# Kernel tuning notes

Hardware: AMD Instinct MI355X
Metric: run time of the kernel (lower is better)

The kernel has to match this reference:

```python
import jax, jax.numpy as jnp
import numpy as np

B, S, D, H, DH, L, F, V, C = 2, 4096, 768, 12, 64, 2, 3072, 50265, 256
NB = S // C
NEG = -1e9


def layer_norm(x, g, b, eps=1e-5):
    m = jnp.mean(x, -1, keepdims=True)
    v = jnp.mean((x - m) ** 2, -1, keepdims=True)
    return (x - m) * jax.lax.rsqrt(v + eps) * g + b


def _blockify(t):
    # t: [B,H,S,DH] -> [B,H,NB,3C,DH], key blocks (b-1, b, b+1) per query block
    tp = jnp.pad(t, ((0, 0), (0, 0), (C, C), (0, 0)))
    tb = tp.reshape(t.shape[0], t.shape[1], NB + 2, C, DH)
    return jnp.concatenate([tb[:, :, :-2], tb[:, :, 1:-1], tb[:, :, 2:]], axis=3)


def sw_attention(x, mask, Wq, bq, Wk, bk, Wv, bv, Wo, bo):
    Bq = x.shape[0]
    def heads(w, b):
        return (x @ w + b).reshape(Bq, S, H, DH).transpose(0, 2, 1, 3)
    q = heads(Wq, bq) / jnp.sqrt(jnp.float32(DH))
    k = heads(Wk, bk)
    v = heads(Wv, bv)
    qb = q.reshape(Bq, H, NB, C, DH)
    k3, v3 = _blockify(k), _blockify(v)
    scores = jnp.einsum('bhncd,bhnkd->bhnck', qb, k3)  # [B,H,NB,C,3C]
    cc = jnp.arange(C)[:, None]
    kk = jnp.arange(3 * C)[None, :]
    band = (kk >= cc) & (kk <= cc + 2 * C)  # exact |i-j| <= 256 sliding window
    lm = mask.at[:, 0].set(0.0)  # global (CLS) key handled separately, not in band
    mp = jnp.pad(lm, ((0, 0), (C, C))).reshape(Bq, NB + 2, C)
    m3 = jnp.concatenate([mp[:, :-2], mp[:, 1:-1], mp[:, 2:]], axis=2)  # [B,NB,3C]
    valid = band[None, None, None] & (m3[:, None, :, None, :] > 0)
    scores = jnp.where(valid, scores, NEG)
    gk, gv = k[:, :, 0, :], v[:, :, 0, :]  # CLS global key/value
    gsc = jnp.einsum('bhncd,bhd->bhnc', qb, gk)[..., None]  # [B,H,NB,C,1]
    gmask = (mask[:, 0] > 0).reshape(Bq, 1, 1, 1, 1)
    gsc = jnp.where(gmask, gsc, NEG)
    probs = jax.nn.softmax(jnp.concatenate([scores, gsc], -1), -1)
    ctx = (jnp.einsum('bhnck,bhnkd->bhncd', probs[..., :3 * C], v3)
           + probs[..., 3 * C:] * gv[:, :, None, None, :])
    ctx = ctx.reshape(Bq, H, S, DH)
    # CLS is a global query: full attention over all keys
    s0 = jnp.einsum('bhd,bhsd->bhs', q[:, :, 0, :], k)
    s0 = jnp.where(mask[:, None, :] > 0, s0, NEG)
    o0 = jnp.einsum('bhs,bhsd->bhd', jax.nn.softmax(s0, -1), v)
    ctx = ctx.at[:, :, 0, :].set(o0)
    out = ctx.transpose(0, 2, 1, 3).reshape(Bq, S, D)
    return out @ Wo + bo


def setup_inputs() -> dict:
    key = jax.random.key(0)
    ks = jax.random.split(key, 16)
    def w(k, shape, s=0.02):
        return (jax.random.normal(k, shape) * s).astype(jnp.float32)
    return {
        'input_ids': jax.random.randint(ks[0], (B, S), 0, V, dtype=jnp.int32),
        'attention_mask': jnp.ones((B, S), dtype=jnp.int32),
        'emb_tok': w(ks[1], (V, D)),
        'emb_pos': w(ks[2], (S, D)),
        'emb_ln_g': jnp.ones((D,), jnp.float32),
        'emb_ln_b': jnp.zeros((D,), jnp.float32),
        'Wq': w(ks[3], (L, D, D)), 'bq': jnp.zeros((L, D), jnp.float32),
        'Wk': w(ks[4], (L, D, D)), 'bk': jnp.zeros((L, D), jnp.float32),
        'Wv': w(ks[5], (L, D, D)), 'bv': jnp.zeros((L, D), jnp.float32),
        'Wo': w(ks[6], (L, D, D)), 'bo': jnp.zeros((L, D), jnp.float32),
        'ln1_g': jnp.ones((L, D), jnp.float32), 'ln1_b': jnp.zeros((L, D), jnp.float32),
        'W1': w(ks[7], (L, D, F)), 'b1': jnp.zeros((L, F), jnp.float32),
        'W2': w(ks[8], (L, F, D)), 'b2': jnp.zeros((L, D), jnp.float32),
        'ln2_g': jnp.ones((L, D), jnp.float32), 'ln2_b': jnp.zeros((L, D), jnp.float32),
        'cls_W': w(ks[9], (D, 3)), 'cls_b': jnp.zeros((3,), jnp.float32),
    }


def reference(input_ids, attention_mask, emb_tok, emb_pos, emb_ln_g, emb_ln_b,
              Wq, bq, Wk, bk, Wv, bv, Wo, bo, ln1_g, ln1_b,
              W1, b1, W2, b2, ln2_g, ln2_b, cls_W, cls_b):
    mask = attention_mask.astype(jnp.float32)
    h = layer_norm(emb_tok[input_ids] + emb_pos[None], emb_ln_g, emb_ln_b)
    for l in range(L):
        a = sw_attention(h, mask, Wq[l], bq[l], Wk[l], bk[l], Wv[l], bv[l], Wo[l], bo[l])
        h = layer_norm(h + a, ln1_g[l], ln1_b[l])
        f = jax.nn.gelu(h @ W1[l] + b1[l], approximate=False) @ W2[l] + b2[l]
        h = layer_norm(h + f, ln2_g[l], ln2_b[l])
    logits = h[:, 0] @ cls_W + cls_b  # dropout is identity at inference
    return logits
```

## Files before the change

### kernel.cpp

```cpp
#include <hip/hip_runtime.h>
#include <math.h>

#define BB 2
#define SS 4096
#define DD 768
#define HH 12
#define LL 2
#define FF 3072
#define CC 256
#define MM 8192
#define QB 128

using frag8 = __attribute__((ext_vector_type(8))) short;
using f32x4 = __attribute__((ext_vector_type(4))) float;

__device__ __forceinline__ unsigned short f2b(float f) {
  unsigned u = __float_as_uint(f);
  u = u + 0x7fffu + ((u >> 16) & 1u);
  return (unsigned short)(u >> 16);
}
__device__ __forceinline__ void unpack8(int4 t, float* f) {
  unsigned u;
  u = (unsigned)t.x; f[0] = __uint_as_float(u << 16); f[1] = __uint_as_float(u & 0xffff0000u);
  u = (unsigned)t.y; f[2] = __uint_as_float(u << 16); f[3] = __uint_as_float(u & 0xffff0000u);
  u = (unsigned)t.z; f[4] = __uint_as_float(u << 16); f[5] = __uint_as_float(u & 0xffff0000u);
  u = (unsigned)t.w; f[6] = __uint_as_float(u << 16); f[7] = __uint_as_float(u & 0xffff0000u);
}
__device__ __forceinline__ void reduce2(float& s1, float& s2) {
#pragma unroll
  for (int off = 32; off > 0; off >>= 1) {
    s1 += __shfl_down(s1, off);
    s2 += __shfl_down(s2, off);
  }
  __shared__ float r1[4], r2[4];
  const int lane = threadIdx.x & 63, wv = threadIdx.x >> 6;
  if (lane == 0) { r1[wv] = s1; r2[wv] = s2; }
  __syncthreads();
  s1 = r1[0] + r1[1] + r1[2] + r1[3];
  s2 = r2[0] + r2[1] + r2[2] + r2[3];
  __syncthreads();
}
__device__ __forceinline__ void async16(const unsigned short* g, unsigned short* l) {
  __builtin_amdgcn_global_load_lds((__attribute__((address_space(1))) void*)(g),
                                   (__attribute__((address_space(3))) void*)(l), 16, 0, 0);
}

__global__ __launch_bounds__(256) void transpose_bf16(const float* __restrict__ in,
                                                      unsigned short* __restrict__ out,
                                                      int K, int N) {
  __shared__ float t[32][33];
  const int n0 = blockIdx.x * 32, k0 = blockIdx.y * 32;
  const int tx = threadIdx.x, ty = threadIdx.y;
#pragma unroll
  for (int i = 0; i < 32; i += 8) t[ty + i][tx] = in[(size_t)(k0 + ty + i) * N + n0 + tx];
  __syncthreads();
#pragma unroll
  for (int i = 0; i < 32; i += 8) out[(size_t)(n0 + ty + i) * K + k0 + tx] = f2b(t[tx][ty + i]);
}

__global__ __launch_bounds__(256) void embed_ln(const int* __restrict__ ids,
                                                const float* __restrict__ etok,
                                                const float* __restrict__ epos,
                                                const float* __restrict__ g,
                                                const float* __restrict__ bb,
                                                float* __restrict__ h32,
                                                unsigned short* __restrict__ hB) {
  const int row = blockIdx.x;
  const int s = row & (SS - 1);
  const int id = ids[row];
  float x[3];
#pragma unroll
  for (int i = 0; i < 3; i++) {
    int j = threadIdx.x + i * 256;
    x[i] = etok[(size_t)id * DD + j] + epos[(size_t)s * DD + j];
  }
  float s1 = x[0] + x[1] + x[2];
  float s2 = x[0] * x[0] + x[1] * x[1] + x[2] * x[2];
  reduce2(s1, s2);
  const float mean = s1 * (1.f / 768.f);
  const float var = s2 * (1.f / 768.f) - mean * mean;
  const float rs = rsqrtf(var + 1e-5f);
#pragma unroll
  for (int i = 0; i < 3; i++) {
    int j = threadIdx.x + i * 256;
    float y = (x[i] - mean) * rs * g[j] + bb[j];
    h32[(size_t)row * DD + j] = y;
    hB[(size_t)row * DD + j] = f2b(y);
  }
}

__global__ __launch_bounds__(256) void ln_res(float* __restrict__ h32,
                                              const float* __restrict__ delta,
                                              const float* __restrict__ g,
                                              const float* __restrict__ bb,
                                              unsigned short* __restrict__ hB) {
  const int row = blockIdx.x;
  float x[3];
#pragma unroll
  for (int i = 0; i < 3; i++) {
    int j = threadIdx.x + i * 256;
    x[i] = h32[(size_t)row * DD + j] + delta[(size_t)row * DD + j];
  }
  float s1 = x[0] + x[1] + x[2];
  float s2 = x[0] * x[0] + x[1] * x[1] + x[2] * x[2];
  reduce2(s1, s2);
  const float mean = s1 * (1.f / 768.f);
  const float var = s2 * (1.f / 768.f) - mean * mean;
  const float rs = rsqrtf(var + 1e-5f);
#pragma unroll
  for (int i = 0; i < 3; i++) {
    int j = threadIdx.x + i * 256;
    float y = (x[i] - mean) * rs * g[j] + bb[j];
    h32[(size_t)row * DD + j] = y;
    hB[(size_t)row * DD + j] = f2b(y);
  }
}

template <int EPI>
__global__ __launch_bounds__(256) void gemm_nt(const unsigned short* __restrict__ A,
                                               const unsigned short* __restrict__ Bt,
                                               const float* __restrict__ bias0,
                                               const float* __restrict__ bias1,
                                               const float* __restrict__ bias2,
                                               float* __restrict__ outF,
                                               unsigned short* __restrict__ oq,
                                               unsigned short* __restrict__ ok,
                                               unsigned short* __restrict__ ov,
                                               int M, int N, int K) {
  __shared__ unsigned short sA[128 * 32];
  __shared__ unsigned short sB[128 * 32];
  const int tid = threadIdx.x;
  const int m0 = blockIdx.y * 128, n0 = blockIdx.x * 128;
  const int wave = tid >> 6, lane = tid & 63;
  const int wm = (wave >> 1) * 64, wn = (wave & 1) * 64;
  const int quad = lane >> 4, r16 = lane & 15;

  const int srow = wave * 32 + (lane >> 2);
  const int scol = (lane & 3) * 8;
  const unsigned short* gA0 = A + (size_t)(m0 + srow) * K + scol;
  const unsigned short* gA1 = gA0 + (size_t)16 * K;
  const unsigned short* gB0 = Bt + (size_t)(n0 + srow) * K + scol;
  const unsigned short* gB1 = gB0 + (size_t)16 * K;
  unsigned short* lA0 = &sA[(wave * 32) * 32];
  unsigned short* lA1 = &sA[(wave * 32 + 16) * 32];
  unsigned short* lB0 = &sB[(wave * 32) * 32];
  unsigned short* lB1 = &sB[(wave * 32 + 16) * 32];

  f32x4 acc[4][4];
#pragma unroll
  for (int i = 0; i < 4; i++)
#pragma unroll
    for (int j = 0; j < 4; j++) acc[i][j] = (f32x4){0.f, 0.f, 0.f, 0.f};

  const int kiters = K >> 5;
  for (int kt = 0; kt < kiters; kt++) {
    const int k0 = kt << 5;
    __syncthreads();
    async16(gA0 + k0, lA0);
    async16(gA1 + k0, lA1);
    async16(gB0 + k0, lB0);
    async16(gB1 + k0, lB1);
    __syncthreads();
    frag8 af[4], bf[4];
#pragma unroll
    for (int i = 0; i < 4; i++)
      af[i] = *reinterpret_cast<const frag8*>(&sA[(wm + i * 16 + r16) * 32 + quad * 8]);
#pragma unroll
    for (int j = 0; j < 4; j++)
      bf[j] = *reinterpret_cast<const frag8*>(&sB[(wn + j * 16 + r16) * 32 + quad * 8]);
#pragma unroll
    for (int i = 0; i < 4; i++)
#pragma unroll
      for (int j = 0; j < 4; j++)
        acc[i][j] = __builtin_amdgcn_mfma_f32_16x16x32_bf16(af[i], bf[j], acc[i][j], 0, 0, 0);
  }

#pragma unroll
  for (int i = 0; i < 4; i++)
#pragma unroll
    for (int j = 0; j < 4; j++)
#pragma unroll
      for (int rr = 0; rr < 4; rr++) {
        const int row = m0 + wm + i * 16 + quad * 4 + rr;
        const int col = n0 + wn + j * 16 + r16;
        if (EPI == 0) {
          outF[(size_t)row * N + col] = acc[i][j][rr] + bias0[col];
        } else if (EPI == 1) {
          const int which = col / 768;
          const int hd = col - which * 768;
          const float bsv = (which == 0) ? bias0[hd] : (which == 1) ? bias1[hd] : bias2[hd];
          float v = acc[i][j][rr] + bsv;
          if (which == 0) v *= 0.125f;
          unsigned short* dst = (which == 0) ? oq : (which == 1) ? ok : ov;
          const int bq = row >> 12, sq = row & (SS - 1);
          dst[((size_t)(bq * HH + (hd >> 6)) * SS + sq) * 64 + (hd & 63)] = f2b(v);
        } else {
          float v = acc[i][j][rr] + bias0[col];
          float ge = 0.5f * v * (1.f + erff(v * 0.70710678118654752f));
          oq[(size_t)row * N + col] = f2b(ge);
        }
      }
}

__global__ __launch_bounds__(256) void attn_win(const unsigned short* __restrict__ qB,
                                                const unsigned short* __restrict__ kB,
                                                const unsigned short* __restrict__ vB,
                                                const int* __restrict__ mask,
                                                unsigned short* __restrict__ ctxB) {
  const int n = blockIdx.x, h = blockIdx.y, b = blockIdx.z;
  const int tid = threadIdx.x;
  const int wave = tid >> 6, lane = tid & 63;
  const int quad = lane >> 4, r16 = lane & 15;
  const size_t headBase = ((size_t)(b * HH + h)) * SS;

  __shared__ unsigned short sK[64 * 72];
  __shared__ unsigned short sVt[64 * 72];
  __shared__ unsigned short sP[4][32 * 72];
  __shared__ int sM[64];

  const int qw0 = n * QB + wave * 32;

  frag8 qf[2][2];
#pragma unroll
  for (int mt = 0; mt < 2; mt++)
#pragma unroll
    for (int kh = 0; kh < 2; kh++) {
      int4 t = *reinterpret_cast<const int4*>(
          qB + (headBase + qw0 + mt * 16 + r16) * 64 + kh * 32 + quad * 8);
      qf[mt][kh] = *reinterpret_cast<frag8*>(&t);
    }

  f32x4 oacc[2][4];
#pragma unroll
  for (int mt = 0; mt < 2; mt++)
#pragma unroll
    for (int dt = 0; dt < 4; dt++) oacc[mt][dt] = (f32x4){0.f, 0.f, 0.f, 0.f};
  float mx[2][4], li[2][4];
#pragma unroll
  for (int mt = 0; mt < 2; mt++)
#pragma unroll
    for (int rr = 0; rr < 4; rr++) { mx[mt][rr] = -1e30f; li[mt][rr] = 0.f; }

  const int kbase = n * QB - 256;
  for (int ch = -1; ch < 10; ch++) {
    const int kc = kbase + ch * 64;
    const bool isG = (ch < 0);
    __syncthreads();
    {
      const int key = tid >> 2, d0 = (tid & 3) * 16;
      const int kp = isG ? ((key == 0) ? 0 : -1) : kc + key;
      int4 a = make_int4(0, 0, 0, 0), c = make_int4(0, 0, 0, 0);
      if (kp >= 0 && kp < SS) {
        const unsigned short* src = kB + (headBase + kp) * 64 + d0;
        a = *reinterpret_cast<const int4*>(src);
        c = *reinterpret_cast<const int4*>(src + 8);
      }
      *reinterpret_cast<int4*>(&sK[key * 72 + d0]) = a;
      *reinterpret_cast<int4*>(&sK[key * 72 + d0 + 8]) = c;
    }
    {
      const int key = tid & 63, d0 = (tid >> 6) * 16;
      const int kp = isG ? ((key == 0) ? 0 : -1) : kc + key;
      int4 a = make_int4(0, 0, 0, 0), c = make_int4(0, 0, 0, 0);
      if (kp >= 0 && kp < SS) {
        const unsigned short* src = vB + (headBase + kp) * 64 + d0;
        a = *reinterpret_cast<const int4*>(src);
        c = *reinterpret_cast<const int4*>(src + 8);
      }
      unsigned short e[16];
      *reinterpret_cast<int4*>(&e[0]) = a;
      *reinterpret_cast<int4*>(&e[8]) = c;
#pragma unroll
      for (int j = 0; j < 16; j++) sVt[(d0 + j) * 72 + key] = e[j];
    }
    if (tid < 64) {
      int ok;
      if (isG) ok = (tid == 0) ? mask[(size_t)b * SS] : 0;
      else {
        const int kp = kc + tid;
        ok = (kp >= 1 && kp < SS) ? mask[(size_t)b * SS + kp] : 0;
      }
      sM[tid] = ok;
    }
    __syncthreads();

    if (!isG && (kc > qw0 + 31 + 256 || kc + 63 < qw0 - 256)) continue;

    f32x4 sacc[2][4];
#pragma unroll
    for (int mt = 0; mt < 2; mt++)
#pragma unroll
      for (int nt = 0; nt < 4; nt++) sacc[mt][nt] = (f32x4){0.f, 0.f, 0.f, 0.f};
#pragma unroll
    for (int kh = 0; kh < 2; kh++) {
      frag8 kf[4];
#pragma unroll
      for (int nt = 0; nt < 4; nt++)
        kf[nt] = *reinterpret_cast<const frag8*>(&sK[(nt * 16 + r16) * 72 + kh * 32 + quad * 8]);
#pragma unroll
      for (int mt = 0; mt < 2; mt++)
#pragma unroll
        for (int nt = 0; nt < 4; nt++)
          sacc[mt][nt] = __builtin_amdgcn_mfma_f32_16x16x32_bf16(qf[mt][kh], kf[nt], sacc[mt][nt], 0, 0, 0);
    }

    int mreg[4];
#pragma unroll
    for (int nt = 0; nt < 4; nt++) mreg[nt] = sM[nt * 16 + r16];
    float al[2][4];
#pragma unroll
    for (int mt = 0; mt < 2; mt++) {
      float rmax[4] = {-1e30f, -1e30f, -1e30f, -1e30f};
#pragma unroll
      for (int nt = 0; nt < 4; nt++) {
        const int kp = isG ? 0 : kc + nt * 16 + r16;
#pragma unroll
        for (int rr = 0; rr < 4; rr++) {
          const int sq = qw0 + mt * 16 + quad * 4 + rr;
          const bool valid = (mreg[nt] != 0) && (isG || (unsigned)(kp - sq + 256) <= 512u);
          const float sv = valid ? sacc[mt][nt][rr] : -1e30f;
          sacc[mt][nt][rr] = sv;
          rmax[rr] = fmaxf(rmax[rr], sv);
        }
      }
#pragma unroll
      for (int rr = 0; rr < 4; rr++) {
#pragma unroll
        for (int off = 1; off < 16; off <<= 1)
          rmax[rr] = fmaxf(rmax[rr], __shfl_xor(rmax[rr], off, 64));
        const float mnew = fmaxf(mx[mt][rr], rmax[rr]);
        al[mt][rr] = __expf(mx[mt][rr] - mnew);
        mx[mt][rr] = mnew;
      }
      float rsum[4] = {0.f, 0.f, 0.f, 0.f};
#pragma unroll
      for (int nt = 0; nt < 4; nt++)
#pragma unroll
        for (int rr = 0; rr < 4; rr++) {
          const float sv = sacc[mt][nt][rr];
          const float p = (sv < -5e29f) ? 0.f : __expf(sv - mx[mt][rr]);
          rsum[rr] += p;
          sP[wave][(mt * 16 + quad * 4 + rr) * 72 + nt * 16 + r16] = f2b(p);
        }
#pragma unroll
      for (int rr = 0; rr < 4; rr++) {
#pragma unroll
        for (int off = 1; off < 16; off <<= 1) rsum[rr] += __shfl_xor(rsum[rr], off, 64);
        li[mt][rr] = li[mt][rr] * al[mt][rr] + rsum[rr];
      }
#pragma unroll
      for (int dt = 0; dt < 4; dt++)
#pragma unroll
        for (int rr = 0; rr < 4; rr++) oacc[mt][dt][rr] *= al[mt][rr];
    }

#pragma unroll
    for (int kh = 0; kh < 2; kh++) {
      frag8 pf[2], vf[4];
#pragma unroll
      for (int mt = 0; mt < 2; mt++)
        pf[mt] = *reinterpret_cast<const frag8*>(&sP[wave][(mt * 16 + r16) * 72 + kh * 32 + quad * 8]);
#pragma unroll
      for (int dt = 0; dt < 4; dt++)
        vf[dt] = *reinterpret_cast<const frag8*>(&sVt[(dt * 16 + r16) * 72 + kh * 32 + quad * 8]);
#pragma unroll
      for (int mt = 0; mt < 2; mt++)
#pragma unroll
        for (int dt = 0; dt < 4; dt++)
          oacc[mt][dt] = __builtin_amdgcn_mfma_f32_16x16x32_bf16(pf[mt], vf[dt], oacc[mt][dt], 0, 0, 0);
    }
  }

#pragma unroll
  for (int mt = 0; mt < 2; mt++) {
    float rli[4];
#pragma unroll
    for (int rr = 0; rr < 4; rr++) rli[rr] = 1.f / li[mt][rr];
#pragma unroll
    for (int dt = 0; dt < 4; dt++)
#pragma unroll
      for (int rr = 0; rr < 4; rr++) {
        const int sq = qw0 + mt * 16 + quad * 4 + rr;
        const int d = dt * 16 + r16;
        ctxB[((size_t)(b * SS + sq)) * DD + h * 64 + d] = f2b(oacc[mt][dt][rr] * rli[rr]);
      }
  }
}

__global__ __launch_bounds__(256) void attn_r0_part(const unsigned short* __restrict__ qB,
                                                    const unsigned short* __restrict__ kB,
                                                    const unsigned short* __restrict__ vB,
                                                    const int* __restrict__ mask,
                                                    float* __restrict__ part) {
  const int ch = blockIdx.x, h = blockIdx.y, b = blockIdx.z;
  const int tid = threadIdx.x;
  const int lane = tid & 63, wave = tid >> 6;
  const size_t headBase = ((size_t)(b * HH + h)) * SS;

  __shared__ float sQ[64];
  __shared__ float wmx[4], wls[4];
  __shared__ float sO[4][64];
  if (tid < 8) {
    int4 t = *reinterpret_cast<const int4*>(qB + headBase * 64 + tid * 8);
    float f[8]; unpack8(t, f);
#pragma unroll
    for (int j = 0; j < 8; j++) sQ[tid * 8 + j] = f[j];
  }
  __syncthreads();

  const int key = ch * 256 + tid;
  float vreg[64];
  float sc;
  {
    float s = 0.f;
    const unsigned short* kp = kB + (headBase + key) * 64;
#pragma unroll
    for (int i = 0; i < 8; i++) {
      int4 t = *reinterpret_cast<const int4*>(kp + i * 8);
      float f[8]; unpack8(t, f);
#pragma unroll
      for (int j = 0; j < 8; j++) s = fmaf(sQ[i * 8 + j], f[j], s);
    }
    sc = (mask[(size_t)b * SS + key] != 0) ? s : -1e9f;
  }
  float m = sc;
#pragma unroll
  for (int off = 1; off < 64; off <<= 1) m = fmaxf(m, __shfl_xor(m, off, 64));
  if (lane == 0) wmx[wave] = m;
  __syncthreads();
  const float Mx = fmaxf(fmaxf(wmx[0], wmx[1]), fmaxf(wmx[2], wmx[3]));
  const float p = __expf(sc - Mx);
  float ls = p;
#pragma unroll
  for (int off = 1; off < 64; off <<= 1) ls += __shfl_xor(ls, off, 64);
  {
    const unsigned short* vp = vB + (headBase + key) * 64;
#pragma unroll
    for (int i = 0; i < 8; i++) {
      int4 t = *reinterpret_cast<const int4*>(vp + i * 8);
      float f[8]; unpack8(t, f);
#pragma unroll
      for (int j = 0; j < 8; j++) vreg[i * 8 + j] = p * f[j];
    }
  }
#pragma unroll
  for (int off = 1; off < 64; off <<= 1)
#pragma unroll
    for (int d = 0; d < 64; d++) vreg[d] += __shfl_xor(vreg[d], off, 64);
  if (lane == 0) {
    wls[wave] = ls;
#pragma unroll
    for (int d = 0; d < 64; d++) sO[wave][d] = vreg[d];
  }
  __syncthreads();
  if (tid < 64) {
    float* pp = part + ((size_t)((b * HH + h) * 16 + ch)) * 68;
    pp[tid] = sO[0][tid] + sO[1][tid] + sO[2][tid] + sO[3][tid];
    if (tid == 0) {
      pp[64] = Mx;
      pp[65] = wls[0] + wls[1] + wls[2] + wls[3];
    }
  }
}

__global__ __launch_bounds__(64) void attn_r0_comb(const float* __restrict__ part,
                                                   unsigned short* __restrict__ ctxB) {
  const int h = blockIdx.x, b = blockIdx.y;
  const int tid = threadIdx.x;
  const float* base = part + ((size_t)((b * HH + h) * 16)) * 68;
  float M = -1e30f;
#pragma unroll
  for (int c = 0; c < 16; c++) M = fmaxf(M, base[c * 68 + 64]);
  float L = 0.f, o = 0.f;
#pragma unroll
  for (int c = 0; c < 16; c++) {
    const float w = __expf(base[c * 68 + 64] - M);
    L += base[c * 68 + 65] * w;
    o = fmaf(w, base[c * 68 + tid], o);
  }
  ctxB[((size_t)(b * SS)) * DD + h * 64 + tid] = f2b(o / L);
}

__global__ __launch_bounds__(256) void cls_head(const float* __restrict__ h32,
                                                const float* __restrict__ W,
                                                const float* __restrict__ bc,
                                                float* __restrict__ out) {
  const int b = blockIdx.x;
  const float* hr = h32 + (size_t)b * SS * DD;
  float p0 = 0.f, p1 = 0.f, p2 = 0.f;
  for (int d = threadIdx.x; d < DD; d += 256) {
    const float x = hr[d];
    p0 = fmaf(x, W[d * 3 + 0], p0);
    p1 = fmaf(x, W[d * 3 + 1], p1);
    p2 = fmaf(x, W[d * 3 + 2], p2);
  }
  __shared__ float r0[256], r1[256], r2[256];
  r0[threadIdx.x] = p0; r1[threadIdx.x] = p1; r2[threadIdx.x] = p2;
  __syncthreads();
  if (threadIdx.x == 0) {
    float s0 = 0.f, s1 = 0.f, s2 = 0.f;
    for (int t = 0; t < 256; t++) { s0 += r0[t]; s1 += r1[t]; s2 += r2[t]; }
    out[b * 3 + 0] = s0 + bc[0];
    out[b * 3 + 1] = s1 + bc[1];
    out[b * 3 + 2] = s2 + bc[2];
  }
}

static const size_t OFF_WT = 0;
static const size_t OFF_H32 = 28311552;
static const size_t OFF_HB = 53477376;
static const size_t OFF_Q = 66060288;
static const size_t OFF_K = 78643200;
static const size_t OFF_V = 91226112;
static const size_t OFF_CTX = 103809024;
static const size_t OFF_DELTA = 116391936;
static const size_t OFF_F1 = 141557760;
static const size_t WS_NEEDED = 191889408;

extern "C" void kernel_launch(void* const* d_in, const int* in_sizes, int n_in,
                              void* d_out, int out_size, void* d_ws, size_t ws_size,
                              hipStream_t stream) {
  (void)in_sizes; (void)n_in; (void)out_size;
  if (ws_size < WS_NEEDED) return;

  const int* ids = (const int*)d_in[0];
  const int* mask = (const int*)d_in[1];
  const float* emb_tok = (const float*)d_in[2];
  const float* emb_pos = (const float*)d_in[3];
  const float* eg = (const float*)d_in[4];
  const float* eb = (const float*)d_in[5];
  const float* Wq = (const float*)d_in[6];
  const float* bq = (const float*)d_in[7];
  const float* Wk = (const float*)d_in[8];
  const float* bk = (const float*)d_in[9];
  const float* Wv = (const float*)d_in[10];
  const float* bv = (const float*)d_in[11];
  const float* Wo = (const float*)d_in[12];
  const float* bo = (const float*)d_in[13];
  const float* ln1g = (const float*)d_in[14];
  const float* ln1b = (const float*)d_in[15];
  const float* W1 = (const float*)d_in[16];
  const float* b1 = (const float*)d_in[17];
  const float* W2 = (const float*)d_in[18];
  const float* b2 = (const float*)d_in[19];
  const float* ln2g = (const float*)d_in[20];
  const float* ln2b = (const float*)d_in[21];
  const float* clsW = (const float*)d_in[22];
  const float* clsb = (const float*)d_in[23];
  float* out = (float*)d_out;

  char* ws = (char*)d_ws;
  unsigned short* wt = (unsigned short*)(ws + OFF_WT);
  float* h32 = (float*)(ws + OFF_H32);
  unsigned short* hB = (unsigned short*)(ws + OFF_HB);
  unsigned short* qb16 = (unsigned short*)(ws + OFF_Q);
  unsigned short* kb16 = (unsigned short*)(ws + OFF_K);
  unsigned short* vb16 = (unsigned short*)(ws + OFF_V);
  unsigned short* ctxB = (unsigned short*)(ws + OFF_CTX);
  float* delta = (float*)(ws + OFF_DELTA);
  unsigned short* f1B = (unsigned short*)(ws + OFF_F1);

  for (int l = 0; l < 2; l++) {
    const size_t lw = (size_t)l * 7077888;
    transpose_bf16<<<dim3(24, 24), dim3(32, 8), 0, stream>>>(Wq + (size_t)l * 589824, wt + lw + 0, 768, 768);
    transpose_bf16<<<dim3(24, 24), dim3(32, 8), 0, stream>>>(Wk + (size_t)l * 589824, wt + lw + 589824, 768, 768);
    transpose_bf16<<<dim3(24, 24), dim3(32, 8), 0, stream>>>(Wv + (size_t)l * 589824, wt + lw + 1179648, 768, 768);
    transpose_bf16<<<dim3(24, 24), dim3(32, 8), 0, stream>>>(Wo + (size_t)l * 589824, wt + lw + 1769472, 768, 768);
    transpose_bf16<<<dim3(96, 24), dim3(32, 8), 0, stream>>>(W1 + (size_t)l * 2359296, wt + lw + 2359296, 768, 3072);
    transpose_bf16<<<dim3(24, 96), dim3(32, 8), 0, stream>>>(W2 + (size_t)l * 2359296, wt + lw + 4718592, 3072, 768);
  }

  embed_ln<<<MM, 256, 0, stream>>>(ids, emb_tok, emb_pos, eg, eb, h32, hB);

  for (int l = 0; l < 2; l++) {
    const size_t lw = (size_t)l * 7077888;
    gemm_nt<1><<<dim3(18, 64), 256, 0, stream>>>(hB, wt + lw, bq + l * 768, bk + l * 768,
                                                 bv + l * 768, nullptr, qb16, kb16, vb16,
                                                 MM, 2304, 768);
    attn_win<<<dim3(SS / QB, 12, 2), 256, 0, stream>>>(qb16, kb16, vb16, mask, ctxB);
    attn_r0_part<<<dim3(16, 12, 2), 256, 0, stream>>>(qb16, kb16, vb16, mask, delta);
    attn_r0_comb<<<dim3(12, 2), 64, 0, stream>>>(delta, ctxB);
    gemm_nt<0><<<dim3(6, 64), 256, 0, stream>>>(ctxB, wt + lw + 1769472, bo + l * 768, nullptr,
                                                nullptr, delta, nullptr, nullptr, nullptr,
                                                MM, 768, 768);
    ln_res<<<MM, 256, 0, stream>>>(h32, delta, ln1g + l * 768, ln1b + l * 768, hB);
    gemm_nt<2><<<dim3(24, 64), 256, 0, stream>>>(hB, wt + lw + 2359296, b1 + l * 3072, nullptr,
                                                 nullptr, nullptr, f1B, nullptr, nullptr,
                                                 MM, 3072, 768);
    gemm_nt<0><<<dim3(6, 64), 256, 0, stream>>>(f1B, wt + lw + 4718592, b2 + l * 768, nullptr,
                                                nullptr, delta, nullptr, nullptr, nullptr,
                                                MM, 768, 3072);
    ln_res<<<MM, 256, 0, stream>>>(h32, delta, ln2g + l * 768, ln2b + l * 768, hB);
  }

  cls_head<<<dim3(BB), 256, 0, stream>>>(h32, clsW, clsb, out);
}
```

Measured before the change: 1.030 ms.

## Store QKV row-major, transpose attention MFMAs, tanh GELU, simplify global-row attention

New measurement: 980.8 us. 4.8% less time.

```diff
diff --git a/kernel.cpp b/kernel.cpp
--- a/kernel.cpp
+++ b/kernel.cpp
@@ -10,6 +10,7 @@
 #define CC 256
 #define MM 8192
 #define QB 128
+#define QKVN 2304
 
 using frag8 = __attribute__((ext_vector_type(8))) short;
 using f32x4 = __attribute__((ext_vector_type(4))) float;
@@ -18,6 +19,12 @@
   unsigned u = __float_as_uint(f);
   u = u + 0x7fffu + ((u >> 16) & 1u);
   return (unsigned short)(u >> 16);
+}
+__device__ __forceinline__ unsigned pack2(float a, float b) {
+  return (unsigned)f2b(a) | ((unsigned)f2b(b) << 16);
+}
+__device__ __forceinline__ float b2f(unsigned short v) {
+  return __uint_as_float(((unsigned)v) << 16);
 }
 __device__ __forceinline__ void unpack8(int4 t, float* f) {
   unsigned u;
@@ -124,8 +131,6 @@
                                                const float* __restrict__ bias2,
                                                float* __restrict__ outF,
                                                unsigned short* __restrict__ oq,
-                                               unsigned short* __restrict__ ok,
-                                               unsigned short* __restrict__ ov,
                                                int M, int N, int K) {
   __shared__ unsigned short sA[128 * 32];
   __shared__ unsigned short sB[128 * 32];
@@ -175,6 +180,11 @@
         acc[i][j] = __builtin_amdgcn_mfma_f32_16x16x32_bf16(af[i], bf[j], acc[i][j], 0, 0, 0);
   }
 
+  const int which = (EPI == 1) ? (n0 / 768) : 0;
+  const float* bw = (EPI == 1) ? ((which == 0) ? bias0 : (which == 1) ? bias1 : bias2) : bias0;
+  const float qsc = (EPI == 1 && which == 0) ? 0.125f : 1.f;
+  const int cofs = which * 768;
+
 #pragma unroll
   for (int i = 0; i < 4; i++)
 #pragma unroll
@@ -186,37 +196,30 @@
         if (EPI == 0) {
           outF[(size_t)row * N + col] = acc[i][j][rr] + bias0[col];
         } else if (EPI == 1) {
-          const int which = col / 768;
-          const int hd = col - which * 768;
-          const float bsv = (which == 0) ? bias0[hd] : (which == 1) ? bias1[hd] : bias2[hd];
-          float v = acc[i][j][rr] + bsv;
-          if (which == 0) v *= 0.125f;
-          unsigned short* dst = (which == 0) ? oq : (which == 1) ? ok : ov;
-          const int bq = row >> 12, sq = row & (SS - 1);
-          dst[((size_t)(bq * HH + (hd >> 6)) * SS + sq) * 64 + (hd & 63)] = f2b(v);
+          float v = (acc[i][j][rr] + bw[col - cofs]) * qsc;
+          oq[(size_t)row * N + col] = f2b(v);
         } else {
           float v = acc[i][j][rr] + bias0[col];
-          float ge = 0.5f * v * (1.f + erff(v * 0.70710678118654752f));
+          float y = 1.5957691216f * (v + 0.044715f * v * v * v);
+          float ge = v / (1.f + __expf(-y));
           oq[(size_t)row * N + col] = f2b(ge);
         }
       }
 }
 
-__global__ __launch_bounds__(256) void attn_win(const unsigned short* __restrict__ qB,
-                                                const unsigned short* __restrict__ kB,
-                                                const unsigned short* __restrict__ vB,
+__global__ __launch_bounds__(256) void attn_win(const unsigned short* __restrict__ qkv,
                                                 const int* __restrict__ mask,
                                                 unsigned short* __restrict__ ctxB) {
   const int n = blockIdx.x, h = blockIdx.y, b = blockIdx.z;
   const int tid = threadIdx.x;
   const int wave = tid >> 6, lane = tid & 63;
   const int quad = lane >> 4, r16 = lane & 15;
-  const size_t headBase = ((size_t)(b * HH + h)) * SS;
+  const size_t rowB = (size_t)(b * SS);
 
   __shared__ unsigned short sK[64 * 72];
   __shared__ unsigned short sVt[64 * 72];
-  __shared__ unsigned short sP[4][32 * 72];
-  __shared__ int sM[64];
+  __shared__ unsigned short sP2[4][32 * 72];
+  __shared__ __align__(16) int sM[64];
 
   const int qw0 = n * QB + wave * 32;
 
@@ -226,20 +229,18 @@
 #pragma unroll
     for (int kh = 0; kh < 2; kh++) {
       int4 t = *reinterpret_cast<const int4*>(
-          qB + (headBase + qw0 + mt * 16 + r16) * 64 + kh * 32 + quad * 8);
+          qkv + (rowB + qw0 + mt * 16 + r16) * QKVN + h * 64 + kh * 32 + quad * 8);
       qf[mt][kh] = *reinterpret_cast<frag8*>(&t);
     }
 
-  f32x4 oacc[2][4];
-#pragma unroll
-  for (int mt = 0; mt < 2; mt++)
-#pragma unroll
-    for (int dt = 0; dt < 4; dt++) oacc[mt][dt] = (f32x4){0.f, 0.f, 0.f, 0.f};
-  float mx[2][4], li[2][4];
-#pragma unroll
-  for (int mt = 0; mt < 2; mt++)
-#pragma unroll
-    for (int rr = 0; rr < 4; rr++) { mx[mt][rr] = -1e30f; li[mt][rr] = 0.f; }
+  f32x4 oacc[4][2];
+#pragma unroll
+  for (int dt = 0; dt < 4; dt++)
+#pragma unroll
+    for (int mt = 0; mt < 2; mt++) oacc[dt][mt] = (f32x4){0.f, 0.f, 0.f, 0.f};
+  float mx[2], li[2];
+#pragma unroll
+  for (int mt = 0; mt < 2; mt++) { mx[mt] = -1e30f; li[mt] = 0.f; }
 
   const int kbase = n * QB - 256;
   for (int ch = -1; ch < 10; ch++) {
@@ -251,7 +252,7 @@
       const int kp = isG ? ((key == 0) ? 0 : -1) : kc + key;
       int4 a = make_int4(0, 0, 0, 0), c = make_int4(0, 0, 0, 0);
       if (kp >= 0 && kp < SS) {
-        const unsigned short* src = kB + (headBase + kp) * 64 + d0;
+        const unsigned short* src = qkv + (rowB + kp) * QKVN + 768 + h * 64 + d0;
         a = *reinterpret_cast<const int4*>(src);
         c = *reinterpret_cast<const int4*>(src + 8);
       }
@@ -263,7 +264,7 @@
       const int kp = isG ? ((key == 0) ? 0 : -1) : kc + key;
       int4 a = make_int4(0, 0, 0, 0), c = make_int4(0, 0, 0, 0);
       if (kp >= 0 && kp < SS) {
-        const unsigned short* src = vB + (headBase + kp) * 64 + d0;
+        const unsigned short* src = qkv + (rowB + kp) * QKVN + 1536 + h * 64 + d0;
         a = *reinterpret_cast<const int4*>(src);
         c = *reinterpret_cast<const int4*>(src + 8);
       }
@@ -275,10 +276,10 @@
     }
     if (tid < 64) {
       int ok;
-      if (isG) ok = (tid == 0) ? mask[(size_t)b * SS] : 0;
+      if (isG) ok = (tid == 0) ? mask[rowB] : 0;
       else {
         const int kp = kc + tid;
-        ok = (kp >= 1 && kp < SS) ? mask[(size_t)b * SS + kp] : 0;
+        ok = (kp >= 1 && kp < SS) ? mask[rowB + kp] : 0;
       }
       sM[tid] = ok;
     }
@@ -286,11 +287,11 @@
 
     if (!isG && (kc > qw0 + 31 + 256 || kc + 63 < qw0 - 256)) continue;
 
-    f32x4 sacc[2][4];
-#pragma unroll
-    for (int mt = 0; mt < 2; mt++)
-#pragma unroll
-      for (int nt = 0; nt < 4; nt++) sacc[mt][nt] = (f32x4){0.f, 0.f, 0.f, 0.f};
+    f32x4 sacc[4][2];
+#pragma unroll
+    for (int nt = 0; nt < 4; nt++)
+#pragma unroll
+      for (int mt = 0; mt < 2; mt++) sacc[nt][mt] = (f32x4){0.f, 0.f, 0.f, 0.f};
 #pragma unroll
     for (int kh = 0; kh < 2; kh++) {
       frag8 kf[4];
@@ -298,110 +299,109 @@
       for (int nt = 0; nt < 4; nt++)
         kf[nt] = *reinterpret_cast<const frag8*>(&sK[(nt * 16 + r16) * 72 + kh * 32 + quad * 8]);
 #pragma unroll
-      for (int mt = 0; mt < 2; mt++)
-#pragma unroll
-        for (int nt = 0; nt < 4; nt++)
-          sacc[mt][nt] = __builtin_amdgcn_mfma_f32_16x16x32_bf16(qf[mt][kh], kf[nt], sacc[mt][nt], 0, 0, 0);
-    }
-
-    int mreg[4];
-#pragma unroll
-    for (int nt = 0; nt < 4; nt++) mreg[nt] = sM[nt * 16 + r16];
-    float al[2][4];
+      for (int nt = 0; nt < 4; nt++)
+#pragma unroll
+        for (int mt = 0; mt < 2; mt++)
+          sacc[nt][mt] = __builtin_amdgcn_mfma_f32_16x16x32_bf16(kf[nt], qf[mt][kh], sacc[nt][mt], 0, 0, 0);
+    }
+
+    int mv[4][4];
+#pragma unroll
+    for (int nt = 0; nt < 4; nt++) {
+      int4 t = *reinterpret_cast<const int4*>(&sM[nt * 16 + quad * 4]);
+      mv[nt][0] = t.x; mv[nt][1] = t.y; mv[nt][2] = t.z; mv[nt][3] = t.w;
+    }
+
 #pragma unroll
     for (int mt = 0; mt < 2; mt++) {
-      float rmax[4] = {-1e30f, -1e30f, -1e30f, -1e30f};
+      const int qg = qw0 + mt * 16 + r16;
+      float m_c = -1e30f;
+#pragma unroll
+      for (int nt = 0; nt < 4; nt++)
+#pragma unroll
+        for (int rr = 0; rr < 4; rr++) {
+          const int kp = kc + nt * 16 + quad * 4 + rr;
+          const bool valid = (mv[nt][rr] != 0) && (isG || (unsigned)(kp - qg + 256) <= 512u);
+          const float s = valid ? sacc[nt][mt][rr] : -1e30f;
+          sacc[nt][mt][rr] = s;
+          m_c = fmaxf(m_c, s);
+        }
+      m_c = fmaxf(m_c, __shfl_xor(m_c, 16, 64));
+      m_c = fmaxf(m_c, __shfl_xor(m_c, 32, 64));
+      const float mnew = fmaxf(mx[mt], m_c);
+      const float alpha = __expf(mx[mt] - mnew);
+      mx[mt] = mnew;
+      float s_c = 0.f;
 #pragma unroll
       for (int nt = 0; nt < 4; nt++) {
-        const int kp = isG ? 0 : kc + nt * 16 + r16;
+        float pk[4];
 #pragma unroll
         for (int rr = 0; rr < 4; rr++) {
-          const int sq = qw0 + mt * 16 + quad * 4 + rr;
-          const bool valid = (mreg[nt] != 0) && (isG || (unsigned)(kp - sq + 256) <= 512u);
-          const float sv = valid ? sacc[mt][nt][rr] : -1e30f;
-          sacc[mt][nt][rr] = sv;
-          rmax[rr] = fmaxf(rmax[rr], sv);
+          const float sv = sacc[nt][mt][rr];
+          float p = __expf(sv - mnew);
+          p = (sv > -5e29f) ? p : 0.f;
+          s_c += p;
+          pk[rr] = p;
         }
+        uint2 w;
+        w.x = pack2(pk[0], pk[1]);
+        w.y = pack2(pk[2], pk[3]);
+        *reinterpret_cast<uint2*>(&sP2[wave][(mt * 16 + r16) * 72 + nt * 16 + quad * 4]) = w;
       }
-#pragma unroll
-      for (int rr = 0; rr < 4; rr++) {
-#pragma unroll
-        for (int off = 1; off < 16; off <<= 1)
-          rmax[rr] = fmaxf(rmax[rr], __shfl_xor(rmax[rr], off, 64));
-        const float mnew = fmaxf(mx[mt][rr], rmax[rr]);
-        al[mt][rr] = __expf(mx[mt][rr] - mnew);
-        mx[mt][rr] = mnew;
-      }
-      float rsum[4] = {0.f, 0.f, 0.f, 0.f};
-#pragma unroll
-      for (int nt = 0; nt < 4; nt++)
-#pragma unroll
-        for (int rr = 0; rr < 4; rr++) {
-          const float sv = sacc[mt][nt][rr];
-          const float p = (sv < -5e29f) ? 0.f : __expf(sv - mx[mt][rr]);
-          rsum[rr] += p;
-          sP[wave][(mt * 16 + quad * 4 + rr) * 72 + nt * 16 + r16] = f2b(p);
-        }
-#pragma unroll
-      for (int rr = 0; rr < 4; rr++) {
-#pragma unroll
-        for (int off = 1; off < 16; off <<= 1) rsum[rr] += __shfl_xor(rsum[rr], off, 64);
-        li[mt][rr] = li[mt][rr] * al[mt][rr] + rsum[rr];
-      }
+      s_c += __shfl_xor(s_c, 16, 64);
+      s_c += __shfl_xor(s_c, 32, 64);
+      li[mt] = li[mt] * alpha + s_c;
 #pragma unroll
       for (int dt = 0; dt < 4; dt++)
 #pragma unroll
-        for (int rr = 0; rr < 4; rr++) oacc[mt][dt][rr] *= al[mt][rr];
+        for (int rr = 0; rr < 4; rr++) oacc[dt][mt][rr] *= alpha;
     }
 
 #pragma unroll
     for (int kh = 0; kh < 2; kh++) {
-      frag8 pf[2], vf[4];
-#pragma unroll
-      for (int mt = 0; mt < 2; mt++)
-        pf[mt] = *reinterpret_cast<const frag8*>(&sP[wave][(mt * 16 + r16) * 72 + kh * 32 + quad * 8]);
+      frag8 vf[4], pf[2];
 #pragma unroll
       for (int dt = 0; dt < 4; dt++)
         vf[dt] = *reinterpret_cast<const frag8*>(&sVt[(dt * 16 + r16) * 72 + kh * 32 + quad * 8]);
 #pragma unroll
       for (int mt = 0; mt < 2; mt++)
-#pragma unroll
-        for (int dt = 0; dt < 4; dt++)
-          oacc[mt][dt] = __builtin_amdgcn_mfma_f32_16x16x32_bf16(pf[mt], vf[dt], oacc[mt][dt], 0, 0, 0);
+        pf[mt] = *reinterpret_cast<const frag8*>(&sP2[wave][(mt * 16 + r16) * 72 + kh * 32 + quad * 8]);
+#pragma unroll
+      for (int dt = 0; dt < 4; dt++)
+#pragma unroll
+        for (int mt = 0; mt < 2; mt++)
+          oacc[dt][mt] = __builtin_amdgcn_mfma_f32_16x16x32_bf16(vf[dt], pf[mt], oacc[dt][mt], 0, 0, 0);
     }
   }
 
 #pragma unroll
   for (int mt = 0; mt < 2; mt++) {
-    float rli[4];
-#pragma unroll
-    for (int rr = 0; rr < 4; rr++) rli[rr] = 1.f / li[mt][rr];
-#pragma unroll
-    for (int dt = 0; dt < 4; dt++)
-#pragma unroll
-      for (int rr = 0; rr < 4; rr++) {
-        const int sq = qw0 + mt * 16 + quad * 4 + rr;
-        const int d = dt * 16 + r16;
-        ctxB[((size_t)(b * SS + sq)) * DD + h * 64 + d] = f2b(oacc[mt][dt][rr] * rli[rr]);
-      }
-  }
-}
-
-__global__ __launch_bounds__(256) void attn_r0_part(const unsigned short* __restrict__ qB,
-                                                    const unsigned short* __restrict__ kB,
-                                                    const unsigned short* __restrict__ vB,
+    const float inv = 1.f / li[mt];
+    const int qg = qw0 + mt * 16 + r16;
+#pragma unroll
+    for (int dt = 0; dt < 4; dt++) {
+      uint2 w;
+      w.x = pack2(oacc[dt][mt][0] * inv, oacc[dt][mt][1] * inv);
+      w.y = pack2(oacc[dt][mt][2] * inv, oacc[dt][mt][3] * inv);
+      *reinterpret_cast<uint2*>(ctxB + (rowB + qg) * DD + h * 64 + dt * 16 + quad * 4) = w;
+    }
+  }
+}
+
+__global__ __launch_bounds__(256) void attn_r0_part(const unsigned short* __restrict__ qkv,
                                                     const int* __restrict__ mask,
                                                     float* __restrict__ part) {
   const int ch = blockIdx.x, h = blockIdx.y, b = blockIdx.z;
   const int tid = threadIdx.x;
   const int lane = tid & 63, wave = tid >> 6;
-  const size_t headBase = ((size_t)(b * HH + h)) * SS;
+  const size_t rowB = (size_t)(b * SS);
 
   __shared__ float sQ[64];
   __shared__ float wmx[4], wls[4];
+  __shared__ float sPp[256];
   __shared__ float sO[4][64];
   if (tid < 8) {
-    int4 t = *reinterpret_cast<const int4*>(qB + headBase * 64 + tid * 8);
+    int4 t = *reinterpret_cast<const int4*>(qkv + rowB * QKVN + h * 64 + tid * 8);
     float f[8]; unpack8(t, f);
 #pragma unroll
     for (int j = 0; j < 8; j++) sQ[tid * 8 + j] = f[j];
@@ -409,11 +409,10 @@
   __syncthreads();
 
   const int key = ch * 256 + tid;
-  float vreg[64];
   float sc;
   {
     float s = 0.f;
-    const unsigned short* kp = kB + (headBase + key) * 64;
+    const unsigned short* kp = qkv + (rowB + key) * QKVN + 768 + h * 64;
 #pragma unroll
     for (int i = 0; i < 8; i++) {
       int4 t = *reinterpret_cast<const int4*>(kp + i * 8);
@@ -421,7 +420,7 @@
 #pragma unroll
       for (int j = 0; j < 8; j++) s = fmaf(sQ[i * 8 + j], f[j], s);
     }
-    sc = (mask[(size_t)b * SS + key] != 0) ? s : -1e9f;
+    sc = (mask[rowB + key] != 0) ? s : -1e9f;
   }
   float m = sc;
 #pragma unroll
@@ -433,25 +432,16 @@
   float ls = p;
 #pragma unroll
   for (int off = 1; off < 64; off <<= 1) ls += __shfl_xor(ls, off, 64);
-  {
-    const unsigned short* vp = vB + (headBase + key) * 64;
-#pragma unroll
-    for (int i = 0; i < 8; i++) {
-      int4 t = *reinterpret_cast<const int4*>(vp + i * 8);
-      float f[8]; unpack8(t, f);
-#pragma unroll
-      for (int j = 0; j < 8; j++) vreg[i * 8 + j] = p * f[j];
-    }
-  }
-#pragma unroll
-  for (int off = 1; off < 64; off <<= 1)
-#pragma unroll
-    for (int d = 0; d < 64; d++) vreg[d] += __shfl_xor(vreg[d], off, 64);
-  if (lane == 0) {
-    wls[wave] = ls;
-#pragma unroll
-    for (int d = 0; d < 64; d++) sO[wave][d] = vreg[d];
-  }
+  sPp[tid] = p;
+  if (lane == 0) wls[wave] = ls;
+  __syncthreads();
+
+  float acc = 0.f;
+  const unsigned short* vb = qkv + (rowB + ch * 256 + wave * 64) * QKVN + 1536 + h * 64 + lane;
+#pragma unroll 4
+  for (int t = 0; t < 64; t++)
+    acc = fmaf(sPp[wave * 64 + t], b2f(vb[(size_t)t * QKVN]), acc);
+  sO[wave][lane] = acc;
   __syncthreads();
   if (tid < 64) {
     float* pp = part + ((size_t)((b * HH + h) * 16 + ch)) * 68;
@@ -509,9 +499,7 @@
 static const size_t OFF_WT = 0;
 static const size_t OFF_H32 = 28311552;
 static const size_t OFF_HB = 53477376;
-static const size_t OFF_Q = 66060288;
-static const size_t OFF_K = 78643200;
-static const size_t OFF_V = 91226112;
+static const size_t OFF_QKV = 66060288;
 static const size_t OFF_CTX = 103809024;
 static const size_t OFF_DELTA = 116391936;
 static const size_t OFF_F1 = 141557760;
@@ -553,9 +541,7 @@
   unsigned short* wt = (unsigned short*)(ws + OFF_WT);
   float* h32 = (float*)(ws + OFF_H32);
   unsigned short* hB = (unsigned short*)(ws + OFF_HB);
-  unsigned short* qb16 = (unsigned short*)(ws + OFF_Q);
-  unsigned short* kb16 = (unsigned short*)(ws + OFF_K);
-  unsigned short* vb16 = (unsigned short*)(ws + OFF_V);
+  unsigned short* qkvB = (unsigned short*)(ws + OFF_QKV);
   unsigned short* ctxB = (unsigned short*)(ws + OFF_CTX);
   float* delta = (float*)(ws + OFF_DELTA);
   unsigned short* f1B = (unsigned short*)(ws + OFF_F1);
@@ -575,20 +561,20 @@
   for (int l = 0; l < 2; l++) {
     const size_t lw = (size_t)l * 7077888;
     gemm_nt<1><<<dim3(18, 64), 256, 0, stream>>>(hB, wt + lw, bq + l * 768, bk + l * 768,
-                                                 bv + l * 768, nullptr, qb16, kb16, vb16,
-                                                 MM, 2304, 768);
-    attn_win<<<dim3(SS / QB, 12, 2), 256, 0, stream>>>(qb16, kb16, vb16, mask, ctxB);
-    attn_r0_part<<<dim3(16, 12, 2), 256, 0, stream>>>(qb16, kb16, vb16, mask, delta);
+                                                 bv + l * 768, nullptr, qkvB,
+                                                 MM, QKVN, 768);
+    attn_win<<<dim3(SS / QB, 12, 2), 256, 0, stream>>>(qkvB, mask, ctxB);
+    attn_r0_part<<<dim3(16, 12, 2), 256, 0, stream>>>(qkvB, mask, delta);
     attn_r0_comb<<<dim3(12, 2), 64, 0, stream>>>(delta, ctxB);
     gemm_nt<0><<<dim3(6, 64), 256, 0, stream>>>(ctxB, wt + lw + 1769472, bo + l * 768, nullptr,
-                                                nullptr, delta, nullptr, nullptr, nullptr,
+                                                nullptr, delta, nullptr,
                                                 MM, 768, 768);
     ln_res<<<MM, 256, 0, stream>>>(h32, delta, ln1g + l * 768, ln1b + l * 768, hB);
     gemm_nt<2><<<dim3(24, 64), 256, 0, stream>>>(hB, wt + lw + 2359296, b1 + l * 3072, nullptr,
-                                                 nullptr, nullptr, f1B, nullptr, nullptr,
+                                                 nullptr, nullptr, f1B,
                                                  MM, 3072, 768);
     gemm_nt<0><<<dim3(6, 64), 256, 0, stream>>>(f1B, wt + lw + 4718592, b2 + l * 768, nullptr,
-                                                nullptr, delta, nullptr, nullptr, nullptr,
+                                                nullptr, delta, nullptr,
                                                 MM, 768, 3072);
     ln_res<<<MM, 256, 0, stream>>>(h32, delta, ln2g + l * 768, ln2b + l * 768, hB);
   }
```
